# Optimization experiments

Hardware: AMD Instinct MI355X
Metric: run time of the kernel (lower is better)

## Reference

```python
import jax, jax.numpy as jnp
import numpy as np

B, H, W, DIM = 32, 56, 56, 192
WSZ = 7
HEADS = 8
DK = 32
DV = 32
INNER_K = HEADS * DK  # 256
INNER_V = HEADS * DV  # 256


def setup_inputs() -> dict:
    key = jax.random.key(0)
    ks = jax.random.split(key, 8)
    s = 0.05
    return {
        "x": jax.random.normal(ks[0], (B, H, W, DIM), jnp.float32),
        "Wq": jax.random.normal(ks[1], (DIM, INNER_K), jnp.float32) * s,
        "Wk": jax.random.normal(ks[2], (DIM, INNER_K), jnp.float32) * s,
        "Wv": jax.random.normal(ks[3], (DIM, INNER_V), jnp.float32) * s,
        "Wlocal": jax.random.normal(ks[4], (3, 3, INNER_V, INNER_V), jnp.float32) * s,
        "b_local": jnp.zeros((INNER_V,), jnp.float32),
        "Wout": jax.random.normal(ks[5], (INNER_V, DIM), jnp.float32) * s,
        "b_out": jnp.zeros((DIM,), jnp.float32),
    }


def _window(t, heads, wsz):
    # (b, H, W, heads*d) -> (b*nx*ny, heads, wsz*wsz, d)
    b, h, w, c = t.shape
    d = c // heads
    nx, ny = h // wsz, w // wsz
    t = t.reshape(b, nx, wsz, ny, wsz, heads, d)
    t = t.transpose(0, 1, 3, 5, 2, 4, 6)
    return t.reshape(b * nx * ny, heads, wsz * wsz, d)


def reference(x, Wq, Wk, Wv, Wlocal, b_local, Wout, b_out):
    scale = DK ** (-0.5)
    # 1x1 convs == per-pixel matmuls
    q = jnp.einsum('bhwc,cd->bhwd', x, Wq)
    k = jnp.einsum('bhwc,cd->bhwd', x, Wk)
    v = jnp.einsum('bhwc,cd->bhwd', x, Wv)
    # 3x3 local interactive conv on v (SAME padding)
    local_out = jax.lax.conv_general_dilated(
        v, Wlocal, window_strides=(1, 1), padding='SAME',
        dimension_numbers=('NHWC', 'HWIO', 'NHWC')) + b_local
    # window partition
    qw = _window(q, HEADS, WSZ)
    kw = _window(k, HEADS, WSZ)
    vw = _window(v, HEADS, WSZ)
    dots = jnp.einsum('bhid,bhjd->bhij', qw, kw) * scale  # (B*nx*ny, heads, 49, 49)
    attn = jax.nn.softmax(dots, axis=-1)
    out = jnp.einsum('bhij,bhjd->bhid', attn, vw)
    # window merge: (b*nx*ny, heads, wsz*wsz, d) -> (b, H, W, heads*d)
    nx, ny = H // WSZ, W // WSZ
    out = out.reshape(B, nx, ny, HEADS, WSZ, WSZ, DV)
    out = out.transpose(0, 1, 4, 2, 5, 3, 6).reshape(B, H, W, HEADS * DV)
    out = out + local_out
    out = jnp.einsum('bhwc,cd->bhwd', out, Wout) + b_out
    return out
```

## Files before the change

kernel.cpp:

```cpp
#include <hip/hip_runtime.h>

typedef unsigned short ushort_t;
typedef __bf16  bf16x8 __attribute__((ext_vector_type(8)));
typedef float   f32x4  __attribute__((ext_vector_type(4)));
typedef unsigned short u16x8 __attribute__((ext_vector_type(8)));

#define MFMA16(a,b,c) __builtin_amdgcn_mfma_f32_16x16x32_bf16((a),(b),(c),0,0,0)
#define WAITVM(N) asm volatile("s_waitcnt vmcnt(" #N ")" ::: "memory")
#define BARRIER() do{ __builtin_amdgcn_s_barrier(); asm volatile("" ::: "memory"); }while(0)

static __device__ __forceinline__ ushort_t f2bf(float f){
  __bf16 h = (__bf16)f;
  return __builtin_bit_cast(ushort_t, h);
}
static __device__ __forceinline__ float bf2f(ushort_t b){
  union{unsigned u; float f;} x; x.u = ((unsigned)b)<<16; return x.f;
}
static __device__ __forceinline__ bf16x8 ldg_bf8u(const ushort_t* p){
  u16x8 r = *(const u16x8*)p;
  return __builtin_bit_cast(bf16x8, r);
}
static __device__ __forceinline__ bf16x8 lds_bf8(const ushort_t* p){
  u16x8 r = *(const u16x8*)p;
  return __builtin_bit_cast(bf16x8, r);
}
static __device__ __forceinline__ void gload_lds16(const ushort_t* g, ushort_t* l){
  __builtin_amdgcn_global_load_lds(
      (const __attribute__((address_space(1))) void*)g,
      (__attribute__((address_space(3))) void*)l, 16, 0, 0);
}

__global__ __launch_bounds__(256) void prep_kernel(
    const float* __restrict__ x,
    const float* __restrict__ Wq, const float* __restrict__ Wk,
    const float* __restrict__ Wv, const float* __restrict__ Wl,
    const float* __restrict__ Wo,
    ushort_t* __restrict__ qkvT, ushort_t* __restrict__ wlT,
    ushort_t* __restrict__ woT, ushort_t* __restrict__ xwin)
{
  int idx = blockIdx.x*256 + threadIdx.x;
  if(idx < 147456){
    int n = idx/192, kk = idx%192;
    const float* W = (n < 256) ? Wq : ((n < 512) ? Wk : Wv);
    qkvT[idx] = f2bf(W[kk*256 + (n & 255)]);
  } else if(idx < 147456 + 589824){
    int t2 = idx - 147456;
    int j   = t2 & 7;
    int sl  = (t2 >> 3) & 3;
    int col = (t2 >> 5) & 255;
    int ks  = (t2 >> 13) & 7;
    int tap = t2 >> 16;
    int grp = sl ^ ((col>>1)&3);
    int k = ks*32 + grp*8 + j;
    wlT[t2] = f2bf(Wl[((size_t)tap*256 + k)*256 + col]);
  } else if(idx < 737280 + 49152){
    int t3 = idx - 737280;
    int col = t3/256, kk = t3%256;
    woT[t3] = f2bf(Wo[kk*192 + col]);
  } else {
    int c = idx - 786432;
    int win = c/1536, t = c%1536;
    int row = t/24, cp = t%24;
    u16x8 o = {0,0,0,0,0,0,0,0};
    if(row < 49){
      int b = win>>6, rem = win&63, wy = rem>>3, wx = rem&7;
      size_t base = (size_t)b*3136 + wy*392 + wx*7;
      int sc = cp ^ (row&7);
      const float* src = x + (base + (row/7)*56 + (row%7))*192 + sc*8;
      float4 f0 = *(const float4*)src;
      float4 f1 = *(const float4*)(src+4);
      o[0]=f2bf(f0.x); o[1]=f2bf(f0.y); o[2]=f2bf(f0.z); o[3]=f2bf(f0.w);
      o[4]=f2bf(f1.x); o[5]=f2bf(f1.y); o[6]=f2bf(f1.z); o[7]=f2bf(f1.w);
    }
    *(u16x8*)&xwin[(size_t)c*8] = o;
  }
}

__global__ __launch_bounds__(256,2) void qkvattn_kernel(
    const ushort_t* __restrict__ xwin, const ushort_t* __restrict__ WT,
    ushort_t* __restrict__ vbuf, ushort_t* __restrict__ attnout)
{
  __shared__ ushort_t lds[38912];
  ushort_t* xLds = lds;
  const int tid = threadIdx.x;
  const int w = tid>>6, l = tid&63, lr = l&15, g = l>>4;
  const int bid = blockIdx.x;
  const int win = bid>>1, head = (bid&1)*4 + w;
  const int b = win>>6, rem = win&63, wy = rem>>3, wx = rem&7;
  const size_t base = (size_t)b*3136 + wy*7*56 + wx*7;

  {
    const ushort_t* xsrc = xwin + (size_t)win*12288;
    #pragma unroll
    for(int r=0;r<6;++r)
      gload_lds16(xsrc + (size_t)(tid + r*256)*8,
                  xLds + (size_t)(r*256 + w*64)*8);
  }
  __syncthreads();

  ushort_t* qkBase = lds + 12288 + w*4608;
  ushort_t* vT     = lds + 30720 + w*2048;
  const ushort_t* Wq_ = WT + (size_t)(head*32)*192;
  const ushort_t* Wk_ = WT + (size_t)(256 + head*32)*192;
  const ushort_t* Wv_ = WT + (size_t)(512 + head*32)*192;

  {
    f32x4 aq[4][2], ak[4][2], av[4][2];
    #pragma unroll
    for(int mi=0;mi<4;++mi)
      #pragma unroll
      for(int nj=0;nj<2;++nj){
        f32x4 z={0.f,0.f,0.f,0.f};
        aq[mi][nj]=z; ak[mi][nj]=z; av[mi][nj]=z;
      }
    #pragma unroll
    for(int ks=0; ks<6; ++ks){
      bf16x8 af[4];
      #pragma unroll
      for(int mi=0;mi<4;++mi){
        int row = mi*16 + lr;
        af[mi] = lds_bf8(&xLds[(row*192 + ks*32 + g*8) ^ ((row&7)<<3)]);
      }
      bf16x8 bq[2], bk[2], bv[2];
      #pragma unroll
      for(int nj=0;nj<2;++nj){
        size_t off = (size_t)(nj*16+lr)*192 + ks*32 + g*8;
        bq[nj] = ldg_bf8u(Wq_ + off);
        bk[nj] = ldg_bf8u(Wk_ + off);
        bv[nj] = ldg_bf8u(Wv_ + off);
      }
      #pragma unroll
      for(int nj=0;nj<2;++nj)
        #pragma unroll
        for(int mi=0;mi<4;++mi){
          aq[mi][nj] = MFMA16(af[mi], bq[nj], aq[mi][nj]);
          ak[mi][nj] = MFMA16(af[mi], bk[nj], ak[mi][nj]);
          av[mi][nj] = MFMA16(af[mi], bv[nj], av[mi][nj]);
        }
    }
    #pragma unroll
    for(int mi=0;mi<4;++mi)
      #pragma unroll
      for(int nj=0;nj<2;++nj)
        #pragma unroll
        for(int i=0;i<4;++i){
          int row = mi*16 + g*4 + i, col = nj*16 + lr;
          qkBase[row*36 + col]        = f2bf(aq[mi][nj][i]);
          qkBase[2304 + row*36 + col] = f2bf(ak[mi][nj][i]);
          ushort_t val = f2bf(av[mi][nj][i]);
          vT[(col*64 + row) ^ ((col&7)<<3)] = val;
          if(row < 49)
            vbuf[(base + (row/7)*56 + (row%7))*256 + head*32 + col] = val;
        }
  }

  f32x4 dot[4][4];
  #pragma unroll
  for(int mi=0;mi<4;++mi)
    #pragma unroll
    for(int nj=0;nj<4;++nj){ f32x4 z={0.f,0.f,0.f,0.f}; dot[mi][nj]=z; }
  bf16x8 qf[4], kf[4];
  #pragma unroll
  for(int t=0;t<4;++t){
    qf[t] = lds_bf8(&qkBase[(t*16+lr)*36 + g*8]);
    kf[t] = lds_bf8(&qkBase[2304 + (t*16+lr)*36 + g*8]);
  }
  #pragma unroll
  for(int mi=0;mi<4;++mi)
    #pragma unroll
    for(int nj=0;nj<4;++nj)
      dot[mi][nj] = MFMA16(qf[mi], kf[nj], dot[mi][nj]);

  const float sc = 0.17677669529663687f * 1.4426950408889634f;
  ushort_t* pl = qkBase;
  #pragma unroll
  for(int mi=0;mi<4;++mi)
    #pragma unroll
    for(int nj=0;nj<4;++nj){
      int col = nj*16 + lr;
      #pragma unroll
      for(int i=0;i<4;++i){
        float e = (col < 49) ? exp2f(dot[mi][nj][i]*sc) : 0.f;
        int row = mi*16 + g*4 + i;
        pl[(row*64 + col) ^ ((row&7)<<3)] = f2bf(e);
      }
    }

  u16x8 ones_u = {0x3f80,0x3f80,0x3f80,0x3f80,0x3f80,0x3f80,0x3f80,0x3f80};
  bf16x8 ones8 = __builtin_bit_cast(bf16x8, ones_u);
  f32x4 o[4][2], rsum[4];
  #pragma unroll
  for(int mi=0;mi<4;++mi){
    f32x4 z={0.f,0.f,0.f,0.f};
    o[mi][0]=z; o[mi][1]=z; rsum[mi]=z;
  }
  #pragma unroll
  for(int ks=0;ks<2;++ks){
    bf16x8 pa[4];
    #pragma unroll
    for(int mi=0;mi<4;++mi){
      int row = mi*16 + lr;
      pa[mi] = lds_bf8(&pl[(row*64 + ks*32 + g*8) ^ ((row&7)<<3)]);
    }
    #pragma unroll
    for(int nj=0;nj<2;++nj){
      int d = nj*16 + lr;
      bf16x8 vb = lds_bf8(&vT[(d*64 + ks*32 + g*8) ^ ((d&7)<<3)]);
      #pragma unroll
      for(int mi=0;mi<4;++mi) o[mi][nj] = MFMA16(pa[mi], vb, o[mi][nj]);
    }
    #pragma unroll
    for(int mi=0;mi<4;++mi) rsum[mi] = MFMA16(pa[mi], ones8, rsum[mi]);
  }
  #pragma unroll
  for(int mi=0;mi<4;++mi){
    #pragma unroll
    for(int i=0;i<4;++i){
      int row = mi*16 + g*4 + i;
      if(row < 49){
        size_t pix = base + (row/7)*56 + (row%7);
        float inv = 1.0f / rsum[mi][i];
        #pragma unroll
        for(int nj=0;nj<2;++nj)
          attnout[pix*256 + head*32 + nj*16 + lr] = f2bf(o[mi][nj][i] * inv);
      }
    }
  }
}

__global__ __launch_bounds__(256,2) void conv_kernel(
    const ushort_t* __restrict__ v, const ushort_t* __restrict__ WlT,
    const float* __restrict__ b_local, ushort_t* __restrict__ local_out)
{
  __shared__ ushort_t aBuf[2][256*32];
  __shared__ ushort_t bBuf[3][256*32];
  const int bid = blockIdx.x;
  const int tile = (bid & 7) * 98 + (bid >> 3);
  const int p0 = tile * 128;
  const int tid = threadIdx.x;
  const int l = tid&63, w=tid>>6, wm=w>>1, wn=w&1, lr=l&15, g=l>>4;

  unsigned maskbits[4];
  int pxloc[4];
  #pragma unroll
  for(int mi=0;mi<4;++mi){
    int p = p0 + wm*64 + mi*16 + lr;
    int rem = p % 3136;
    int y = rem/56, x = rem%56;
    unsigned mb = 0;
    #pragma unroll
    for(int tap=0;tap<9;++tap){
      int dy = tap/3 - 1, dx = tap%3 - 1;
      if(((unsigned)(y+dy) < 56u) && ((unsigned)(x+dx) < 56u)) mb |= (1u<<tap);
    }
    maskbits[mi] = mb;
    pxloc[mi] = wm*64 + mi*16 + lr + 64;
  }

  auto stageA = [&](int ks, ushort_t* dst){
    #pragma unroll
    for(int r=0;r<4;++r){
      int c = tid + r*256;
      int px = c>>2, sl = c&3;
      int px_abs = p0 - 64 + px;
      px_abs = min(max(px_abs, 0), 100351);
      int chunk = sl ^ ((px>>1)&3);
      gload_lds16(v + (size_t)px_abs*256 + ks*32 + chunk*8,
                  dst + (size_t)(r*256 + w*64)*8);
    }
  };
  auto stageB = [&](int ks, int tap, ushort_t* dst){
    const ushort_t* src = WlT + ((size_t)tap*8 + ks)*8192;
    #pragma unroll
    for(int r=0;r<4;++r){
      gload_lds16(src + (size_t)(tid + r*256)*8,
                  dst + (size_t)(r*256 + w*64)*8);
    }
  };

  f32x4 acc[4][8];
  #pragma unroll
  for(int mi=0;mi<4;++mi)
    #pragma unroll
    for(int nj=0;nj<8;++nj){ f32x4 z={0.f,0.f,0.f,0.f}; acc[mi][nj]=z; }

  auto compute = [&](int tap, const ushort_t* aL, const ushort_t* bL){
    int shift = (tap/3 - 1)*56 + (tap%3 - 1);
    bf16x8 af[4];
    #pragma unroll
    for(int mi=0;mi<4;++mi){
      int px = pxloc[mi] + shift;
      int sl = g ^ ((px>>1)&3);
      u16x8 rv = *(const u16x8*)&aL[px*32 + sl*8];
      if(!((maskbits[mi]>>tap)&1)){ u16x8 z={0,0,0,0,0,0,0,0}; rv=z; }
      af[mi] = __builtin_bit_cast(bf16x8, rv);
    }
    __builtin_amdgcn_s_setprio(1);
    #pragma unroll
    for(int nj=0;nj<8;++nj){
      int col = wn*128 + nj*16 + lr;
      int slb = g ^ ((col>>1)&3);
      bf16x8 bfr = lds_bf8(&bL[col*32 + slb*8]);
      #pragma unroll
      for(int mi=0;mi<4;++mi) acc[mi][nj] = MFMA16(af[mi], bfr, acc[mi][nj]);
    }
    __builtin_amdgcn_s_setprio(0);
  };

  stageA(0, aBuf[0]);
  stageB(0, 0, bBuf[0]);
  stageB(0, 1, bBuf[1]);

  for(int ks=0; ks<7; ++ks){
    #pragma unroll
    for(int tap=0; tap<9; ++tap){
      if(tap==1) WAITVM(8); else WAITVM(4);
      BARRIER();
      if(tap==0) stageA(ks+1, aBuf[(ks+1)&1]);
      stageB(ks + (tap+2)/9, (tap+2)%9, bBuf[(tap+2)%3]);
      compute(tap, aBuf[ks&1], bBuf[tap%3]);
    }
  }
  #pragma unroll
  for(int tap=0; tap<9; ++tap){
    if(tap==8) WAITVM(0); else WAITVM(4);
    BARRIER();
    if(tap<7) stageB(7, tap+2, bBuf[(tap+2)%3]);
    compute(tap, aBuf[1], bBuf[tap%3]);
  }

  #pragma unroll
  for(int nj=0;nj<8;++nj){
    int col = wn*128 + nj*16 + lr;
    float bb = b_local[col];
    #pragma unroll
    for(int mi=0;mi<4;++mi)
      #pragma unroll
      for(int i=0;i<4;++i){
        int p = p0 + wm*64 + mi*16 + g*4 + i;
        local_out[(size_t)p*256 + col] = f2bf(acc[mi][nj][i] + bb);
      }
  }
}

__global__ __launch_bounds__(256,4) void outproj_kernel(
    const ushort_t* __restrict__ attnout, const ushort_t* __restrict__ locl,
    const ushort_t* __restrict__ WoT, const float* __restrict__ b_out,
    float* __restrict__ out)
{
  __shared__ ushort_t aLds[64*256];
  const int m0 = blockIdx.x * 64;
  const int tid = threadIdx.x;
  const int l = tid&63, w = tid>>6, lr=l&15, g=l>>4;
  #pragma unroll
  for(int r=0;r<8;++r){
    int c = tid + r*256;
    int row = c>>5, cc = c&31;
    size_t off = (size_t)(m0+row)*256 + cc*8;
    u16x8 a = *(const u16x8*)(attnout + off);
    u16x8 b2 = *(const u16x8*)(locl + off);
    u16x8 o;
    #pragma unroll
    for(int j=0;j<8;++j) o[j] = f2bf(bf2f(a[j]) + bf2f(b2[j]));
    *(u16x8*)&aLds[(row*256 + cc*8) ^ ((row&7)<<3)] = o;
  }
  __syncthreads();

  const ushort_t* Wbase = WoT + (size_t)(w*48)*256;
  f32x4 acc[4][3];
  #pragma unroll
  for(int mi=0;mi<4;++mi)
    #pragma unroll
    for(int nj=0;nj<3;++nj){ f32x4 z={0.f,0.f,0.f,0.f}; acc[mi][nj]=z; }

  #pragma unroll
  for(int ks=0;ks<8;++ks){
    bf16x8 bfr[3];
    #pragma unroll
    for(int nj=0;nj<3;++nj)
      bfr[nj] = ldg_bf8u(Wbase + (size_t)(nj*16+lr)*256 + ks*32 + g*8);
    bf16x8 af[4];
    #pragma unroll
    for(int mi=0;mi<4;++mi){
      int row = mi*16 + lr;
      af[mi] = lds_bf8(&aLds[(row*256 + ks*32 + g*8) ^ ((row&7)<<3)]);
    }
    #pragma unroll
    for(int nj=0;nj<3;++nj)
      #pragma unroll
      for(int mi=0;mi<4;++mi) acc[mi][nj] = MFMA16(af[mi], bfr[nj], acc[mi][nj]);
  }
  #pragma unroll
  for(int nj=0;nj<3;++nj){
    int col = w*48 + nj*16 + lr;
    float bb = b_out[col];
    #pragma unroll
    for(int mi=0;mi<4;++mi)
      #pragma unroll
      for(int i=0;i<4;++i){
        int row = mi*16 + g*4 + i;
        out[(size_t)(m0+row)*192 + col] = acc[mi][nj][i] + bb;
      }
  }
}

extern "C" void kernel_launch(void* const* d_in, const int* in_sizes, int n_in,
                              void* d_out, int out_size, void* d_ws, size_t ws_size,
                              hipStream_t stream)
{
  const float* x  = (const float*)d_in[0];
  const float* Wq = (const float*)d_in[1];
  const float* Wk = (const float*)d_in[2];
  const float* Wv = (const float*)d_in[3];
  const float* Wl = (const float*)d_in[4];
  const float* bl = (const float*)d_in[5];
  const float* Wo = (const float*)d_in[6];
  const float* bo = (const float*)d_in[7];
  float* out = (float*)d_out;
  char* ws = (char*)d_ws;
  ushort_t* attnout = (ushort_t*)(ws);
  ushort_t* xwin    = (ushort_t*)(ws + 51380224);
  ushort_t* vbuf    = (ushort_t*)(ws + 102760448);
  ushort_t* locl    = (ushort_t*)(ws + 205520896);
  ushort_t* qkvT    = (ushort_t*)(ws + 256901120);
  ushort_t* wlT     = (ushort_t*)(ws + 257196032);
  ushort_t* woT     = (ushort_t*)(ws + 258375680);

  prep_kernel<<<15360, 256, 0, stream>>>(x, Wq, Wk, Wv, Wl, Wo, qkvT, wlT, woT, xwin);
  qkvattn_kernel<<<4096, 256, 0, stream>>>(xwin, qkvT, vbuf, attnout);
  conv_kernel<<<784, 256, 0, stream>>>(vbuf, wlT, bl, locl);
  outproj_kernel<<<1568, 256, 0, stream>>>(attnout, locl, woT, bo, out);
}
```

Baseline: 305.2 us.

## Fold Wv into local conv weights and convolve bf16 x directly

Precomposes Wv with the 3x3 local conv weights in the prep kernel so the conv runs on a bf16 copy of x with K=192 instead of on v with K=256. The attention kernel no longer writes v to global memory, and the conv kernel loop shrinks from 8 to 6 K-steps. In exchange, prep performs a naive fp32 weight-composition matmul and writes an extra bf16 NHWC copy of x. Rounding also changes, since v is no longer rounded to bf16 before the conv.

```diff
diff --git a/kernel.cpp b/kernel.cpp
--- a/kernel.cpp
+++ b/kernel.cpp
@@ -35,30 +35,21 @@
     const float* __restrict__ Wq, const float* __restrict__ Wk,
     const float* __restrict__ Wv, const float* __restrict__ Wl,
     const float* __restrict__ Wo,
-    ushort_t* __restrict__ qkvT, ushort_t* __restrict__ wlT,
-    ushort_t* __restrict__ woT, ushort_t* __restrict__ xwin)
+    ushort_t* __restrict__ qkvT, ushort_t* __restrict__ woT,
+    ushort_t* __restrict__ xwin, ushort_t* __restrict__ xbf,
+    ushort_t* __restrict__ WcT)
 {
   int idx = blockIdx.x*256 + threadIdx.x;
   if(idx < 147456){
     int n = idx/192, kk = idx%192;
     const float* W = (n < 256) ? Wq : ((n < 512) ? Wk : Wv);
     qkvT[idx] = f2bf(W[kk*256 + (n & 255)]);
-  } else if(idx < 147456 + 589824){
-    int t2 = idx - 147456;
-    int j   = t2 & 7;
-    int sl  = (t2 >> 3) & 3;
-    int col = (t2 >> 5) & 255;
-    int ks  = (t2 >> 13) & 7;
-    int tap = t2 >> 16;
-    int grp = sl ^ ((col>>1)&3);
-    int k = ks*32 + grp*8 + j;
-    wlT[t2] = f2bf(Wl[((size_t)tap*256 + k)*256 + col]);
-  } else if(idx < 737280 + 49152){
-    int t3 = idx - 737280;
+  } else if(idx < 196608){
+    int t3 = idx - 147456;
     int col = t3/256, kk = t3%256;
     woT[t3] = f2bf(Wo[kk*192 + col]);
-  } else {
-    int c = idx - 786432;
+  } else if(idx < 3342336){
+    int c = idx - 196608;
     int win = c/1536, t = c%1536;
     int row = t/24, cp = t%24;
     u16x8 o = {0,0,0,0,0,0,0,0};
@@ -66,19 +57,45 @@
       int b = win>>6, rem = win&63, wy = rem>>3, wx = rem&7;
       size_t base = (size_t)b*3136 + wy*392 + wx*7;
       int sc = cp ^ (row&7);
-      const float* src = x + (base + (row/7)*56 + (row%7))*192 + sc*8;
+      size_t pix = base + (row/7)*56 + (row%7);
+      const float* src = x + pix*192 + sc*8;
       float4 f0 = *(const float4*)src;
       float4 f1 = *(const float4*)(src+4);
       o[0]=f2bf(f0.x); o[1]=f2bf(f0.y); o[2]=f2bf(f0.z); o[3]=f2bf(f0.w);
       o[4]=f2bf(f1.x); o[5]=f2bf(f1.y); o[6]=f2bf(f1.z); o[7]=f2bf(f1.w);
+      *(u16x8*)&xbf[pix*192 + sc*8] = o;
     }
     *(u16x8*)&xwin[(size_t)c*8] = o;
+  } else if(idx < 3452928){
+    int t = idx - 3342336;
+    int o = t & 255;
+    int tc = t >> 8;
+    int tap = tc/48, c4 = tc%48;
+    float acc0=0.f, acc1=0.f, acc2=0.f, acc3=0.f;
+    const float* wlp = Wl + (size_t)tap*65536 + o;
+    const float* wv0 = Wv + (size_t)(c4      )*256;
+    const float* wv1 = Wv + (size_t)(c4 +  48)*256;
+    const float* wv2 = Wv + (size_t)(c4 +  96)*256;
+    const float* wv3 = Wv + (size_t)(c4 + 144)*256;
+    for(int k=0;k<256;++k){
+      float wlv = wlp[(size_t)k*256];
+      acc0 += wv0[k]*wlv; acc1 += wv1[k]*wlv;
+      acc2 += wv2[k]*wlv; acc3 += wv3[k]*wlv;
+    }
+    float accs[4] = {acc0, acc1, acc2, acc3};
+    #pragma unroll
+    for(int i=0;i<4;++i){
+      int c = c4 + i*48;
+      int ks = c>>5, r = c&31, grp = r>>3, j = r&7;
+      int sl = grp ^ ((o>>1)&3);
+      WcT[((size_t)tap*6 + ks)*8192 + o*32 + sl*8 + j] = f2bf(accs[i]);
+    }
   }
 }
 
 __global__ __launch_bounds__(256,2) void qkvattn_kernel(
     const ushort_t* __restrict__ xwin, const ushort_t* __restrict__ WT,
-    ushort_t* __restrict__ vbuf, ushort_t* __restrict__ attnout)
+    ushort_t* __restrict__ attnout)
 {
   __shared__ ushort_t lds[38912];
   ushort_t* xLds = lds;
@@ -147,10 +164,7 @@
           int row = mi*16 + g*4 + i, col = nj*16 + lr;
           qkBase[row*36 + col]        = f2bf(aq[mi][nj][i]);
           qkBase[2304 + row*36 + col] = f2bf(ak[mi][nj][i]);
-          ushort_t val = f2bf(av[mi][nj][i]);
-          vT[(col*64 + row) ^ ((col&7)<<3)] = val;
-          if(row < 49)
-            vbuf[(base + (row/7)*56 + (row%7))*256 + head*32 + col] = val;
+          vT[(col*64 + row) ^ ((col&7)<<3)] = f2bf(av[mi][nj][i]);
         }
   }
 
@@ -229,7 +243,7 @@
 }
 
 __global__ __launch_bounds__(256,2) void conv_kernel(
-    const ushort_t* __restrict__ v, const ushort_t* __restrict__ WlT,
+    const ushort_t* __restrict__ xbf, const ushort_t* __restrict__ WcT,
     const float* __restrict__ b_local, ushort_t* __restrict__ local_out)
 {
   __shared__ ushort_t aBuf[2][256*32];
@@ -265,12 +279,12 @@
       int px_abs = p0 - 64 + px;
       px_abs = min(max(px_abs, 0), 100351);
       int chunk = sl ^ ((px>>1)&3);
-      gload_lds16(v + (size_t)px_abs*256 + ks*32 + chunk*8,
+      gload_lds16(xbf + (size_t)px_abs*192 + ks*32 + chunk*8,
                   dst + (size_t)(r*256 + w*64)*8);
     }
   };
   auto stageB = [&](int ks, int tap, ushort_t* dst){
-    const ushort_t* src = WlT + ((size_t)tap*8 + ks)*8192;
+    const ushort_t* src = WcT + ((size_t)tap*6 + ks)*8192;
     #pragma unroll
     for(int r=0;r<4;++r){
       gload_lds16(src + (size_t)(tid + r*256)*8,
@@ -311,7 +325,7 @@
   stageB(0, 0, bBuf[0]);
   stageB(0, 1, bBuf[1]);
 
-  for(int ks=0; ks<7; ++ks){
+  for(int ks=0; ks<5; ++ks){
     #pragma unroll
     for(int tap=0; tap<9; ++tap){
       if(tap==1) WAITVM(8); else WAITVM(4);
@@ -325,7 +339,7 @@
   for(int tap=0; tap<9; ++tap){
     if(tap==8) WAITVM(0); else WAITVM(4);
     BARRIER();
-    if(tap<7) stageB(7, tap+2, bBuf[(tap+2)%3]);
+    if(tap<7) stageB(5, tap+2, bBuf[(tap+2)%3]);
     compute(tap, aBuf[1], bBuf[tap%3]);
   }
 
@@ -420,14 +434,15 @@
   char* ws = (char*)d_ws;
   ushort_t* attnout = (ushort_t*)(ws);
   ushort_t* xwin    = (ushort_t*)(ws + 51380224);
-  ushort_t* vbuf    = (ushort_t*)(ws + 102760448);
+  ushort_t* xbf     = (ushort_t*)(ws + 102760448);
   ushort_t* locl    = (ushort_t*)(ws + 205520896);
   ushort_t* qkvT    = (ushort_t*)(ws + 256901120);
-  ushort_t* wlT     = (ushort_t*)(ws + 257196032);
+  ushort_t* WcT     = (ushort_t*)(ws + 257196032);
   ushort_t* woT     = (ushort_t*)(ws + 258375680);
 
-  prep_kernel<<<15360, 256, 0, stream>>>(x, Wq, Wk, Wv, Wl, Wo, qkvT, wlT, woT, xwin);
-  qkvattn_kernel<<<4096, 256, 0, stream>>>(xwin, qkvT, vbuf, attnout);
-  conv_kernel<<<784, 256, 0, stream>>>(vbuf, wlT, bl, locl);
+  prep_kernel<<<13488, 256, 0, stream>>>(x, Wq, Wk, Wv, Wl, Wo,
+                                         qkvT, woT, xwin, xbf, WcT);
+  qkvattn_kernel<<<4096, 256, 0, stream>>>(xwin, qkvT, attnout);
+  conv_kernel<<<784, 256, 0, stream>>>(xbf, WcT, bl, locl);
   outproj_kernel<<<1568, 256, 0, stream>>>(attnout, locl, woT, bo, out);
 }
```

After: 311.6 us. 1.02x slower.
